# Kernel optimization log

Measured on AMD Instinct MI355X. Metric: run time of the kernel, lower is better.

Reference implementation:

```python
import jax, jax.numpy as jnp
import numpy as np

E, D, H, K = 8, 1024, 4096, 2  # num_experts, input/output dim, hidden dim, top-k
B, S = 2, 2048


def setup_inputs() -> dict:
    key = jax.random.key(0)
    ks = jax.random.split(key, 5)
    s = 0.02
    return {
        "x": jax.random.normal(ks[0], (B, S, D), dtype=jnp.float32),
        "router_w": jax.random.normal(ks[1], (D, E), dtype=jnp.float32) * s,
        "router_b": jnp.zeros((E,), jnp.float32),
        "w1": jax.random.normal(ks[2], (E, D, H), dtype=jnp.float32) * s,
        "b1": jnp.zeros((E, H), jnp.float32),
        "w2": jax.random.normal(ks[3], (E, H, D), dtype=jnp.float32) * s,
        "b2": jnp.zeros((E, D), jnp.float32),
        "gamma": jnp.ones((E, D), jnp.float32),
        "beta": jnp.zeros((E, D), jnp.float32),
    }


def _layernorm(y, g, b, eps=1e-5):
    mu = y.mean(-1, keepdims=True)
    var = ((y - mu) ** 2).mean(-1, keepdims=True)
    return (y - mu) * jax.lax.rsqrt(var + eps) * g + b


def reference(x, router_w, router_b, w1, b1, w2, b2, gamma, beta):
    # Router
    router_logits = x @ router_w + router_b            # [B,S,E]
    probs = jax.nn.softmax(router_logits, axis=-1)
    topk_p, topk_i = jax.lax.top_k(probs, K)           # [B,S,K]
    topk_p = topk_p / topk_p.sum(-1, keepdims=True)

    # All experts over all tokens (equivalent to the masked dense loop,
    # since every expert op is per-token). Dropout = identity (eval).
    h = jax.nn.gelu(jnp.einsum('bsd,edh->ebsh', x, w1) + b1[:, None, None, :],
                    approximate=False)                  # [E,B,S,H]
    y = jnp.einsum('ebsh,ehd->ebsd', h, w2) + b2[:, None, None, :]
    eo = _layernorm(y + x[None], gamma[:, None, None, :], beta[:, None, None, :])  # [E,B,S,D]

    # Combine top-k experts per token
    eo = jnp.moveaxis(eo, 0, 2)                         # [B,S,E,D]
    gathered = jnp.take_along_axis(eo, topk_i[..., None], axis=2)  # [B,S,K,D]
    output = (gathered * topk_p[..., None]).sum(axis=2)            # [B,S,D]
    return output, router_logits
```

## Files before the change

### kernel.cpp

```cpp
#include <hip/hip_runtime.h>
#include <math.h>

#define NE 8
#define DD 1024
#define HH 4096
#define TT 4096
#define RR 8192

typedef __attribute__((ext_vector_type(8))) short short8;
typedef __attribute__((ext_vector_type(4))) float f32x4;

__device__ __forceinline__ unsigned short f2bf(float f) {
    unsigned int u = __float_as_uint(f);
    u += 0x7fffu + ((u >> 16) & 1u);
    return (unsigned short)(u >> 16);
}

__device__ __forceinline__ float gelu_fast(float v) {
    float z = fabsf(v) * 0.70710678f;
    float t = __fdividef(1.0f, fmaf(0.3275911f, z, 1.0f));
    float p = fmaf(1.061405429f, t, -1.453152027f);
    p = fmaf(p, t, 1.421413741f);
    p = fmaf(p, t, -0.284496736f);
    p = fmaf(p, t, 0.254829592f);
    p = p * t;
    float erf = fmaf(-p, __expf(-z * z), 1.0f);
    return 0.5f * v * (1.0f + copysignf(erf, v));
}

__device__ __forceinline__ void async_copy16(void* lds, const void* g) {
    auto* lp = reinterpret_cast<__attribute__((address_space(3))) unsigned int*>(
        (unsigned int)(unsigned long long)(lds));
    auto* gp = reinterpret_cast<const __attribute__((address_space(1))) unsigned int*>(
        (unsigned long long)(g));
    __builtin_amdgcn_global_load_lds(gp, lp, 16, 0, 0);
}


__global__ void cvtx_kernel(const float* __restrict__ x, unsigned short* __restrict__ xb) {
    size_t i = (size_t)(blockIdx.x * 256 + threadIdx.x) * 4;
    float4 v = *(const float4*)&x[i];
    unsigned int lo = (unsigned int)f2bf(v.x) | ((unsigned int)f2bf(v.y) << 16);
    unsigned int hi = (unsigned int)f2bf(v.z) | ((unsigned int)f2bf(v.w) << 16);
    *(uint2*)&xb[i] = make_uint2(lo, hi);
}

__global__ __launch_bounds__(256) void transpose_swz_kernel(const float* __restrict__ src,
        unsigned short* __restrict__ dst, int K, int N) {
    const int e = blockIdx.z;
    src += (size_t)e * K * N;
    dst += (size_t)e * K * N;
    const int c0 = blockIdx.x * 64;
    const int r0 = blockIdx.y * 64;
    __shared__ unsigned short t[64][65];
    const int tid = threadIdx.x;
    const int rc4 = (tid & 15) * 4, rr = tid >> 4;
    #pragma unroll
    for (int i = 0; i < 4; i++) {
        int r = rr + i * 16;
        float4 v = *(const float4*)&src[(size_t)(r0 + r) * N + c0 + rc4];
        t[r][rc4]     = f2bf(v.x);
        t[r][rc4 + 1] = f2bf(v.y);
        t[r][rc4 + 2] = f2bf(v.z);
        t[r][rc4 + 3] = f2bf(v.w);
    }
    __syncthreads();
    const int n_local = tid & 63;
    const int n = c0 + n_local;
    const int nt = n >> 7, row = n & 127;
    const int Kdiv32 = K >> 5;
    #pragma unroll
    for (int it = 0; it < 2; it++) {
        int dg = (tid >> 6) + 4 * it;
        int kb = 2 * blockIdx.y + (dg >> 2);
        int q = dg & 3;
        unsigned short tmp[8];
        #pragma unroll
        for (int i = 0; i < 8; i++) tmp[i] = t[dg * 8 + i][n_local];
        size_t idx = ((((size_t)nt * Kdiv32 + kb) * 4 + q) * 128 + row) * 8;
        *(uint4*)&dst[idx] = *(uint4*)&tmp[0];
    }
}

__global__ void router_kernel(const float* __restrict__ x, const float* __restrict__ rw,
                              const float* __restrict__ rb, float* __restrict__ logits_out,
                              int* __restrict__ topk_e, float* __restrict__ topk_p,
                              int* __restrict__ counts) {
    const int t = blockIdx.x;
    const int tid = threadIdx.x;
    float4 xv = *(const float4*)&x[(size_t)t * DD + tid * 4];
    const float* rwp = rw + (size_t)(tid * 4) * NE;
    float acc[NE];
    #pragma unroll
    for (int e = 0; e < NE; e++) acc[e] = 0.f;
    float xs[4] = {xv.x, xv.y, xv.z, xv.w};
    #pragma unroll
    for (int i = 0; i < 4; i++) {
        #pragma unroll
        for (int e = 0; e < NE; e++) acc[e] += xs[i] * rwp[i * NE + e];
    }
    #pragma unroll
    for (int e = 0; e < NE; e++) {
        float v = acc[e];
        for (int off = 32; off > 0; off >>= 1) v += __shfl_down(v, off);
        acc[e] = v;
    }
    __shared__ float part[4][NE];
    if ((tid & 63) == 0) {
        #pragma unroll
        for (int e = 0; e < NE; e++) part[tid >> 6][e] = acc[e];
    }
    __syncthreads();
    if (tid == 0) {
        float lg[NE];
        #pragma unroll
        for (int e = 0; e < NE; e++)
            lg[e] = part[0][e] + part[1][e] + part[2][e] + part[3][e] + rb[e];
        #pragma unroll
        for (int e = 0; e < NE; e++) logits_out[(size_t)t * NE + e] = lg[e];
        float m = lg[0];
        #pragma unroll
        for (int e = 1; e < NE; e++) m = fmaxf(m, lg[e]);
        float pr[NE];
        #pragma unroll
        for (int e = 0; e < NE; e++) pr[e] = __expf(lg[e] - m);
        int i0 = 0;
        #pragma unroll
        for (int e = 1; e < NE; e++) if (pr[e] > pr[i0]) i0 = e;
        int i1 = (i0 == 0) ? 1 : 0;
        #pragma unroll
        for (int e = 0; e < NE; e++) if (e != i0 && pr[e] > pr[i1]) i1 = e;
        float p0 = pr[i0], p1 = pr[i1];
        float inv = 1.f / (p0 + p1);
        topk_e[t * 2] = i0;  topk_e[t * 2 + 1] = i1;
        topk_p[t * 2] = p0 * inv;  topk_p[t * 2 + 1] = p1 * inv;
        atomicAdd(&counts[i0], 1);
        atomicAdd(&counts[i1], 1);
    }
}

__global__ void prefix_kernel(const int* __restrict__ counts, int* __restrict__ offs,
                              int* __restrict__ cursor) {
    if (threadIdx.x == 0) {
        int a = 0;
        for (int e = 0; e < NE; e++) { offs[e] = a; cursor[e] = a; a += counts[e]; }
        offs[NE] = a;
    }
}

__global__ void scatter_kernel(const int* __restrict__ topk_e, int* __restrict__ cursor,
                               int* __restrict__ row_token, int* __restrict__ slot_of) {
    int i = blockIdx.x * 256 + threadIdx.x;
    int e = topk_e[i];
    int pos = atomicAdd(&cursor[e], 1);
    row_token[pos] = i >> 1;
    slot_of[i] = pos;
}

__device__ __forceinline__ void mfma_step(const unsigned short* Ab, const unsigned short* Bb,
        int wr, int wc, int m16, int q, f32x4 (&acc)[4][4]) {
    short8 af[4], bfr[4];
    #pragma unroll
    for (int i = 0; i < 4; i++) af[i] = *(const short8*)&Ab[q * 1024 + (wr + i * 16 + m16) * 8];
    #pragma unroll
    for (int j = 0; j < 4; j++) bfr[j] = *(const short8*)&Bb[q * 1024 + (wc + j * 16 + m16) * 8];
    #pragma unroll
    for (int i = 0; i < 4; i++)
        #pragma unroll
        for (int j = 0; j < 4; j++)
            acc[i][j] = __builtin_amdgcn_mfma_f32_16x16x32_bf16(af[i], bfr[j], acc[i][j], 0, 0, 0);
}

template <int NK>
__device__ __forceinline__ void kloop_db(
        const unsigned short* ag0, const unsigned short* ag1, const unsigned short* bg,
        unsigned short* As, unsigned short* Bs,
        int wv, int lane, int wr, int wc, int m16, int q, f32x4 (&acc)[4][4]) {
    unsigned short* alA = As + wv * 1024 + lane * 8;
    unsigned short* blB = Bs + wv * 1024 + lane * 8;

    async_copy16(alA, ag0);        async_copy16(alA + 512, ag1);
    async_copy16(blB, bg);         async_copy16(blB + 512, bg + 512);
    ag0 += 32; ag1 += 32; bg += 4096;

    #pragma unroll 1
    for (int it = 0; it < NK / 2 - 1; ++it) {
        async_copy16(alA + 4096, ag0); async_copy16(alA + 4608, ag1);
        async_copy16(blB + 4096, bg);  async_copy16(blB + 4608, bg + 512);
        ag0 += 32; ag1 += 32; bg += 4096;
        asm volatile("s_waitcnt vmcnt(4)" ::: "memory");
        __builtin_amdgcn_s_barrier();
        mfma_step(As, Bs, wr, wc, m16, q, acc);
        __builtin_amdgcn_s_barrier();
        async_copy16(alA, ag0);        async_copy16(alA + 512, ag1);
        async_copy16(blB, bg);         async_copy16(blB + 512, bg + 512);
        ag0 += 32; ag1 += 32; bg += 4096;
        asm volatile("s_waitcnt vmcnt(4)" ::: "memory");
        __builtin_amdgcn_s_barrier();
        mfma_step(As + 4096, Bs + 4096, wr, wc, m16, q, acc);
        __builtin_amdgcn_s_barrier();
    }
    async_copy16(alA + 4096, ag0); async_copy16(alA + 4608, ag1);
    async_copy16(blB + 4096, bg);  async_copy16(blB + 4608, bg + 512);
    asm volatile("s_waitcnt vmcnt(4)" ::: "memory");
    __builtin_amdgcn_s_barrier();
    mfma_step(As, Bs, wr, wc, m16, q, acc);
    asm volatile("s_waitcnt vmcnt(0)" ::: "memory");
    __builtin_amdgcn_s_barrier();
    mfma_step(As + 4096, Bs + 4096, wr, wc, m16, q, acc);
}

__global__ __launch_bounds__(256) void gemm1_kernel(
        const unsigned short* __restrict__ xb, const unsigned short* __restrict__ w1s,
        const float* __restrict__ b1, const int* __restrict__ offs,
        const int* __restrict__ row_token, unsigned short* __restrict__ hbuf) {
    const int bid = blockIdx.x;
    const int xcd = bid & 7;
    const int mem = (bid >> 3) & 7;
    const int g   = (bid >> 6) * 8 + xcd;
    const int nth = g & 3;
    const int rt  = (g >> 2) & 31;
    const int e   = g >> 7;
    const int nt  = nth * 8 + mem;

    const int r0 = offs[e];
    const int ne = offs[e + 1] - r0;
    if (rt * 128 >= ne) return;

    __shared__ __align__(16) unsigned short As[2][4096];
    __shared__ __align__(16) unsigned short Bs[2][4096];

    const int tid = threadIdx.x;
    const int lane = tid & 63;
    const int wv = tid >> 6;
    const int wr = (wv >> 1) * 64, wc = (wv & 1) * 64;
    const int m16 = lane & 15, q = lane >> 4;

    int ra = rt * 128 + lane;       ra = ra < ne ? ra : ne - 1;
    int rb = rt * 128 + 64 + lane;  rb = rb < ne ? rb : ne - 1;
    const unsigned short* ag0 = xb + (size_t)row_token[r0 + ra] * DD + wv * 8;
    const unsigned short* ag1 = xb + (size_t)row_token[r0 + rb] * DD + wv * 8;

    const unsigned short* bg = w1s + (size_t)e * HH * DD + (size_t)nt * (DD >> 5) * 4096
                               + wv * 1024 + lane * 8;

    f32x4 acc[4][4];
    f32x4 zero = {0.f, 0.f, 0.f, 0.f};
    #pragma unroll
    for (int i = 0; i < 4; i++)
        #pragma unroll
        for (int j = 0; j < 4; j++) acc[i][j] = zero;

    kloop_db<DD / 32>(ag0, ag1, bg, &As[0][0], &Bs[0][0], wv, lane, wr, wc, m16, q, acc);

    const int n0 = nt * 128;
    float b1v[4];
    #pragma unroll
    for (int j = 0; j < 4; j++) b1v[j] = b1[(size_t)e * HH + n0 + wc + j * 16 + m16];
    #pragma unroll
    for (int i = 0; i < 4; i++) {
        #pragma unroll
        for (int rg = 0; rg < 4; rg++) {
            int rr = rt * 128 + wr + i * 16 + q * 4 + rg;
            if (rr < ne) {
                unsigned short* hrow = hbuf + (size_t)(r0 + rr) * HH;
                #pragma unroll
                for (int j = 0; j < 4; j++) {
                    int col = n0 + wc + j * 16 + m16;
                    float v = acc[i][j][rg] + b1v[j];
                    hrow[col] = f2bf(gelu_fast(v));
                }
            }
        }
    }
}

__global__ __launch_bounds__(256) void gemm2_kernel(
        const unsigned short* __restrict__ hbuf, const unsigned short* __restrict__ w2s,
        const float* __restrict__ b2, const float* __restrict__ x,
        const int* __restrict__ offs, const int* __restrict__ row_token,
        float* __restrict__ yp0, float* __restrict__ yp1) {
    const int bid = blockIdx.x;
    const int xcd = bid & 7;
    const int nt  = (bid >> 3) & 7;
    const int g   = (bid >> 6) * 8 + xcd;
    const int chunk = g & 1;
    const int rt  = (g >> 1) & 31;
    const int e   = g >> 6;

    const int r0 = offs[e];
    const int ne = offs[e + 1] - r0;
    if (rt * 128 >= ne) return;
    const int kbase = chunk * (HH / 2);
    float* ybuf = chunk ? yp1 : yp0;

    __shared__ __align__(16) unsigned short As[2][4096];
    __shared__ __align__(16) unsigned short Bs[2][4096];

    const int tid = threadIdx.x;
    const int lane = tid & 63;
    const int wv = tid >> 6;
    const int wr = (wv >> 1) * 64, wc = (wv & 1) * 64;
    const int m16 = lane & 15, q = lane >> 4;

    int ra = rt * 128 + lane;       ra = ra < ne ? ra : ne - 1;
    int rb = rt * 128 + 64 + lane;  rb = rb < ne ? rb : ne - 1;
    const unsigned short* ag0 = hbuf + (size_t)(r0 + ra) * HH + kbase + wv * 8;
    const unsigned short* ag1 = hbuf + (size_t)(r0 + rb) * HH + kbase + wv * 8;

    const unsigned short* bg = w2s + (size_t)e * DD * HH + (size_t)nt * (HH >> 5) * 4096
                               + (size_t)(kbase >> 5) * 4096 + wv * 1024 + lane * 8;

    f32x4 acc[4][4];
    f32x4 zero = {0.f, 0.f, 0.f, 0.f};
    #pragma unroll
    for (int i = 0; i < 4; i++)
        #pragma unroll
        for (int j = 0; j < 4; j++) acc[i][j] = zero;

    kloop_db<(HH / 2) / 32>(ag0, ag1, bg, &As[0][0], &Bs[0][0], wv, lane, wr, wc, m16, q, acc);

    const int n0 = nt * 128;
    float b2v[4] = {0.f, 0.f, 0.f, 0.f};
    if (chunk == 0) {
        #pragma unroll
        for (int j = 0; j < 4; j++) b2v[j] = b2[(size_t)e * DD + n0 + wc + j * 16 + m16];
    }
    #pragma unroll
    for (int i = 0; i < 4; i++) {
        #pragma unroll
        for (int rg = 0; rg < 4; rg++) {
            int rr = rt * 128 + wr + i * 16 + q * 4 + rg;
            if (rr < ne) {
                float* yrow = ybuf + (size_t)(r0 + rr) * DD;
                if (chunk == 0) {
                    int tok = row_token[r0 + rr];
                    const float* xrow = x + (size_t)tok * DD;
                    #pragma unroll
                    for (int j = 0; j < 4; j++) {
                        int col = n0 + wc + j * 16 + m16;
                        yrow[col] = acc[i][j][rg] + b2v[j] + xrow[col];
                    }
                } else {
                    #pragma unroll
                    for (int j = 0; j < 4; j++) {
                        int col = n0 + wc + j * 16 + m16;
                        yrow[col] = acc[i][j][rg];
                    }
                }
            }
        }
    }
}

__global__ void ln_combine_kernel(const float* __restrict__ yp0, const float* __restrict__ yp1,
                                  const int* __restrict__ slot_of,
                                  const int* __restrict__ topk_e, const float* __restrict__ topk_p,
                                  const float* __restrict__ gamma, const float* __restrict__ beta,
                                  float* __restrict__ out) {
    const int t = blockIdx.x;
    const int tid = threadIdx.x;
    __shared__ float ps[8];
    float4 o = {0.f, 0.f, 0.f, 0.f};
    #pragma unroll
    for (int k = 0; k < 2; k++) {
        int row = slot_of[t * 2 + k];
        int e = topk_e[t * 2 + k];
        float p = topk_p[t * 2 + k];
        float4 v0 = *(const float4*)&yp0[(size_t)row * DD + tid * 4];
        float4 v1 = *(const float4*)&yp1[(size_t)row * DD + tid * 4];
        float4 v = {v0.x + v1.x, v0.y + v1.y, v0.z + v1.z, v0.w + v1.w};
        float s = v.x + v.y + v.z + v.w;
        float sq = v.x * v.x + v.y * v.y + v.z * v.z + v.w * v.w;
        for (int off = 32; off > 0; off >>= 1) {
            s += __shfl_down(s, off);
            sq += __shfl_down(sq, off);
        }
        if ((tid & 63) == 0) { ps[tid >> 6] = s; ps[4 + (tid >> 6)] = sq; }
        __syncthreads();
        float fs = ps[0] + ps[1] + ps[2] + ps[3];
        float fq = ps[4] + ps[5] + ps[6] + ps[7];
        float mu = fs * (1.0f / DD);
        float var = fq * (1.0f / DD) - mu * mu;
        float rsig = rsqrtf(var + 1e-5f);
        float4 g = *(const float4*)&gamma[(size_t)e * DD + tid * 4];
        float4 bb = *(const float4*)&beta[(size_t)e * DD + tid * 4];
        o.x += p * ((v.x - mu) * rsig * g.x + bb.x);
        o.y += p * ((v.y - mu) * rsig * g.y + bb.y);
        o.z += p * ((v.z - mu) * rsig * g.z + bb.z);
        o.w += p * ((v.w - mu) * rsig * g.w + bb.w);
        __syncthreads();
    }
    *(float4*)&out[(size_t)t * DD + tid * 4] = o;
}

extern "C" void kernel_launch(void* const* d_in, const int* in_sizes, int n_in,
                              void* d_out, int out_size, void* d_ws, size_t ws_size,
                              hipStream_t stream) {
    const float* x     = (const float*)d_in[0];
    const float* rw    = (const float*)d_in[1];
    const float* rb    = (const float*)d_in[2];
    const float* w1    = (const float*)d_in[3];
    const float* b1    = (const float*)d_in[4];
    const float* w2    = (const float*)d_in[5];
    const float* b2    = (const float*)d_in[6];
    const float* gamma = (const float*)d_in[7];
    const float* beta  = (const float*)d_in[8];

    float* out    = (float*)d_out;
    float* logits = out + (size_t)TT * DD;

    char* w = (char*)d_ws;
    int*   counts    = (int*)(w + 0);
    int*   offs      = (int*)(w + 64);
    int*   cursor    = (int*)(w + 128);
    int*   topk_e    = (int*)(w + 4096);
    float* topk_p    = (float*)(w + 36864);
    int*   row_token = (int*)(w + 69632);
    int*   slot_of   = (int*)(w + 102400);
    unsigned short* xb   = (unsigned short*)(w + (size_t)1 * 1048576);
    unsigned short* w1s  = (unsigned short*)(w + (size_t)9 * 1048576);
    unsigned short* w2s  = (unsigned short*)(w + (size_t)73 * 1048576);
    unsigned short* hbuf = (unsigned short*)(w + (size_t)137 * 1048576);
    float*          yp0  = (float*)(w + (size_t)1 * 1048576);
    float*          yp1  = (float*)(w + (size_t)33 * 1048576);

    hipMemsetAsync(w, 0, 1024, stream);

    transpose_swz_kernel<<<dim3(HH / 64, DD / 64, NE), 256, 0, stream>>>(w1, w1s, DD, HH);
    transpose_swz_kernel<<<dim3(DD / 64, HH / 64, NE), 256, 0, stream>>>(w2, w2s, HH, DD);
    cvtx_kernel<<<4096, 256, 0, stream>>>(x, xb);
    router_kernel<<<TT, 256, 0, stream>>>(x, rw, rb, logits, topk_e, topk_p, counts);
    prefix_kernel<<<1, 64, 0, stream>>>(counts, offs, cursor);
    scatter_kernel<<<RR / 256, 256, 0, stream>>>(topk_e, cursor, row_token, slot_of);
    gemm1_kernel<<<32 * 32 * NE, 256, 0, stream>>>(xb, w1s, b1, offs, row_token, hbuf);
    gemm2_kernel<<<16 * 32 * NE, 256, 0, stream>>>(hbuf, w2s, b2, x, offs, row_token, yp0, yp1);
    ln_combine_kernel<<<TT, 256, 0, stream>>>(yp0, yp1, slot_of, topk_e, topk_p, gamma, beta, out);
}
```

Measured before the change: 750.7 us.

## Use triple-buffered LDS pipeline and drop split-K in second GEMM

Replaces the double-buffered K loop with a three-stage async-copy ring buffer, so two tiles are in flight while one is being multiplied, which should hide more global-load latency. It also removes the two-way split-K in gemm2: each block now covers the full hidden dimension and writes a single y buffer, and ln_combine reads one partial instead of two. This cuts the fp32 partial-buffer traffic, but it halves gemm2's grid and raises LDS use per block (48KB), which may reduce occupancy and parallelism.

```diff
diff --git a/kernel.cpp b/kernel.cpp
--- a/kernel.cpp
+++ b/kernel.cpp
@@ -172,42 +172,41 @@
 }
 
 template <int NK>
-__device__ __forceinline__ void kloop_db(
+__device__ __forceinline__ void kloop_3s(
         const unsigned short* ag0, const unsigned short* ag1, const unsigned short* bg,
         unsigned short* As, unsigned short* Bs,
         int wv, int lane, int wr, int wc, int m16, int q, f32x4 (&acc)[4][4]) {
     unsigned short* alA = As + wv * 1024 + lane * 8;
     unsigned short* blB = Bs + wv * 1024 + lane * 8;
 
-    async_copy16(alA, ag0);        async_copy16(alA + 512, ag1);
-    async_copy16(blB, bg);         async_copy16(blB + 512, bg + 512);
-    ag0 += 32; ag1 += 32; bg += 4096;
-
+    #pragma unroll
+    for (int p = 0; p < 2; ++p) {
+        async_copy16(alA + p * 4096, ag0); async_copy16(alA + p * 4096 + 512, ag1);
+        async_copy16(blB + p * 4096, bg);  async_copy16(blB + p * 4096 + 512, bg + 512);
+        ag0 += 32; ag1 += 32; bg += 4096;
+    }
+
+    int cOff = 0;
+    int sOff = 2 * 4096;
     #pragma unroll 1
-    for (int it = 0; it < NK / 2 - 1; ++it) {
-        async_copy16(alA + 4096, ag0); async_copy16(alA + 4608, ag1);
-        async_copy16(blB + 4096, bg);  async_copy16(blB + 4608, bg + 512);
+    for (int t = 0; t < NK - 2; ++t) {
+        async_copy16(alA + sOff, ag0); async_copy16(alA + sOff + 512, ag1);
+        async_copy16(blB + sOff, bg);  async_copy16(blB + sOff + 512, bg + 512);
         ag0 += 32; ag1 += 32; bg += 4096;
-        asm volatile("s_waitcnt vmcnt(4)" ::: "memory");
+        asm volatile("s_waitcnt vmcnt(8)" ::: "memory");
         __builtin_amdgcn_s_barrier();
-        mfma_step(As, Bs, wr, wc, m16, q, acc);
+        mfma_step(As + cOff, Bs + cOff, wr, wc, m16, q, acc);
         __builtin_amdgcn_s_barrier();
-        async_copy16(alA, ag0);        async_copy16(alA + 512, ag1);
-        async_copy16(blB, bg);         async_copy16(blB + 512, bg + 512);
-        ag0 += 32; ag1 += 32; bg += 4096;
-        asm volatile("s_waitcnt vmcnt(4)" ::: "memory");
-        __builtin_amdgcn_s_barrier();
-        mfma_step(As + 4096, Bs + 4096, wr, wc, m16, q, acc);
-        __builtin_amdgcn_s_barrier();
-    }
-    async_copy16(alA + 4096, ag0); async_copy16(alA + 4608, ag1);
-    async_copy16(blB + 4096, bg);  async_copy16(blB + 4608, bg + 512);
+        sOff = cOff;
+        cOff += 4096; if (cOff == 3 * 4096) cOff = 0;
+    }
     asm volatile("s_waitcnt vmcnt(4)" ::: "memory");
     __builtin_amdgcn_s_barrier();
-    mfma_step(As, Bs, wr, wc, m16, q, acc);
+    mfma_step(As + cOff, Bs + cOff, wr, wc, m16, q, acc);
+    cOff += 4096; if (cOff == 3 * 4096) cOff = 0;
     asm volatile("s_waitcnt vmcnt(0)" ::: "memory");
     __builtin_amdgcn_s_barrier();
-    mfma_step(As + 4096, Bs + 4096, wr, wc, m16, q, acc);
+    mfma_step(As + cOff, Bs + cOff, wr, wc, m16, q, acc);
 }
 
 __global__ __launch_bounds__(256) void gemm1_kernel(
@@ -227,8 +226,8 @@
     const int ne = offs[e + 1] - r0;
     if (rt * 128 >= ne) return;
 
-    __shared__ __align__(16) unsigned short As[2][4096];
-    __shared__ __align__(16) unsigned short Bs[2][4096];
+    __shared__ __align__(16) unsigned short As[3][4096];
+    __shared__ __align__(16) unsigned short Bs[3][4096];
 
     const int tid = threadIdx.x;
     const int lane = tid & 63;
@@ -251,7 +250,7 @@
         #pragma unroll
         for (int j = 0; j < 4; j++) acc[i][j] = zero;
 
-    kloop_db<DD / 32>(ag0, ag1, bg, &As[0][0], &Bs[0][0], wv, lane, wr, wc, m16, q, acc);
+    kloop_3s<DD / 32>(ag0, ag1, bg, &As[0][0], &Bs[0][0], wv, lane, wr, wc, m16, q, acc);
 
     const int n0 = nt * 128;
     float b1v[4];
@@ -279,23 +278,20 @@
         const unsigned short* __restrict__ hbuf, const unsigned short* __restrict__ w2s,
         const float* __restrict__ b2, const float* __restrict__ x,
         const int* __restrict__ offs, const int* __restrict__ row_token,
-        float* __restrict__ yp0, float* __restrict__ yp1) {
+        float* __restrict__ yp) {
     const int bid = blockIdx.x;
     const int xcd = bid & 7;
     const int nt  = (bid >> 3) & 7;
     const int g   = (bid >> 6) * 8 + xcd;
-    const int chunk = g & 1;
-    const int rt  = (g >> 1) & 31;
-    const int e   = g >> 6;
+    const int rt  = g & 31;
+    const int e   = g >> 5;
 
     const int r0 = offs[e];
     const int ne = offs[e + 1] - r0;
     if (rt * 128 >= ne) return;
-    const int kbase = chunk * (HH / 2);
-    float* ybuf = chunk ? yp1 : yp0;
-
-    __shared__ __align__(16) unsigned short As[2][4096];
-    __shared__ __align__(16) unsigned short Bs[2][4096];
+
+    __shared__ __align__(16) unsigned short As[3][4096];
+    __shared__ __align__(16) unsigned short Bs[3][4096];
 
     const int tid = threadIdx.x;
     const int lane = tid & 63;
@@ -305,11 +301,11 @@
 
     int ra = rt * 128 + lane;       ra = ra < ne ? ra : ne - 1;
     int rb = rt * 128 + 64 + lane;  rb = rb < ne ? rb : ne - 1;
-    const unsigned short* ag0 = hbuf + (size_t)(r0 + ra) * HH + kbase + wv * 8;
-    const unsigned short* ag1 = hbuf + (size_t)(r0 + rb) * HH + kbase + wv * 8;
+    const unsigned short* ag0 = hbuf + (size_t)(r0 + ra) * HH + wv * 8;
+    const unsigned short* ag1 = hbuf + (size_t)(r0 + rb) * HH + wv * 8;
 
     const unsigned short* bg = w2s + (size_t)e * DD * HH + (size_t)nt * (HH >> 5) * 4096
-                               + (size_t)(kbase >> 5) * 4096 + wv * 1024 + lane * 8;
+                               + wv * 1024 + lane * 8;
 
     f32x4 acc[4][4];
     f32x4 zero = {0.f, 0.f, 0.f, 0.f};
@@ -318,42 +314,32 @@
         #pragma unroll
         for (int j = 0; j < 4; j++) acc[i][j] = zero;
 
-    kloop_db<(HH / 2) / 32>(ag0, ag1, bg, &As[0][0], &Bs[0][0], wv, lane, wr, wc, m16, q, acc);
+    kloop_3s<HH / 32>(ag0, ag1, bg, &As[0][0], &Bs[0][0], wv, lane, wr, wc, m16, q, acc);
 
     const int n0 = nt * 128;
-    float b2v[4] = {0.f, 0.f, 0.f, 0.f};
-    if (chunk == 0) {
-        #pragma unroll
-        for (int j = 0; j < 4; j++) b2v[j] = b2[(size_t)e * DD + n0 + wc + j * 16 + m16];
-    }
+    float b2v[4];
+    #pragma unroll
+    for (int j = 0; j < 4; j++) b2v[j] = b2[(size_t)e * DD + n0 + wc + j * 16 + m16];
     #pragma unroll
     for (int i = 0; i < 4; i++) {
         #pragma unroll
         for (int rg = 0; rg < 4; rg++) {
             int rr = rt * 128 + wr + i * 16 + q * 4 + rg;
             if (rr < ne) {
-                float* yrow = ybuf + (size_t)(r0 + rr) * DD;
-                if (chunk == 0) {
-                    int tok = row_token[r0 + rr];
-                    const float* xrow = x + (size_t)tok * DD;
-                    #pragma unroll
-                    for (int j = 0; j < 4; j++) {
-                        int col = n0 + wc + j * 16 + m16;
-                        yrow[col] = acc[i][j][rg] + b2v[j] + xrow[col];
-                    }
-                } else {
-                    #pragma unroll
-                    for (int j = 0; j < 4; j++) {
-                        int col = n0 + wc + j * 16 + m16;
-                        yrow[col] = acc[i][j][rg];
-                    }
+                float* yrow = yp + (size_t)(r0 + rr) * DD;
+                int tok = row_token[r0 + rr];
+                const float* xrow = x + (size_t)tok * DD;
+                #pragma unroll
+                for (int j = 0; j < 4; j++) {
+                    int col = n0 + wc + j * 16 + m16;
+                    yrow[col] = acc[i][j][rg] + b2v[j] + xrow[col];
                 }
             }
         }
     }
 }
 
-__global__ void ln_combine_kernel(const float* __restrict__ yp0, const float* __restrict__ yp1,
+__global__ void ln_combine_kernel(const float* __restrict__ yp,
                                   const int* __restrict__ slot_of,
                                   const int* __restrict__ topk_e, const float* __restrict__ topk_p,
                                   const float* __restrict__ gamma, const float* __restrict__ beta,
@@ -367,9 +353,7 @@
         int row = slot_of[t * 2 + k];
         int e = topk_e[t * 2 + k];
         float p = topk_p[t * 2 + k];
-        float4 v0 = *(const float4*)&yp0[(size_t)row * DD + tid * 4];
-        float4 v1 = *(const float4*)&yp1[(size_t)row * DD + tid * 4];
-        float4 v = {v0.x + v1.x, v0.y + v1.y, v0.z + v1.z, v0.w + v1.w};
+        float4 v = *(const float4*)&yp[(size_t)row * DD + tid * 4];
         float s = v.x + v.y + v.z + v.w;
         float sq = v.x * v.x + v.y * v.y + v.z * v.z + v.w * v.w;
         for (int off = 32; off > 0; off >>= 1) {
@@ -422,8 +406,7 @@
     unsigned short* w1s  = (unsigned short*)(w + (size_t)9 * 1048576);
     unsigned short* w2s  = (unsigned short*)(w + (size_t)73 * 1048576);
     unsigned short* hbuf = (unsigned short*)(w + (size_t)137 * 1048576);
-    float*          yp0  = (float*)(w + (size_t)1 * 1048576);
-    float*          yp1  = (float*)(w + (size_t)33 * 1048576);
+    float*          yp   = (float*)(w + (size_t)1 * 1048576);
 
     hipMemsetAsync(w, 0, 1024, stream);
 
@@ -434,6 +417,6 @@
     prefix_kernel<<<1, 64, 0, stream>>>(counts, offs, cursor);
     scatter_kernel<<<RR / 256, 256, 0, stream>>>(topk_e, cursor, row_token, slot_of);
     gemm1_kernel<<<32 * 32 * NE, 256, 0, stream>>>(xb, w1s, b1, offs, row_token, hbuf);
-    gemm2_kernel<<<16 * 32 * NE, 256, 0, stream>>>(hbuf, w2s, b2, x, offs, row_token, yp0, yp1);
-    ln_combine_kernel<<<TT, 256, 0, stream>>>(yp0, yp1, slot_of, topk_e, topk_p, gamma, beta, out);
-}
+    gemm2_kernel<<<8 * 32 * NE, 256, 0, stream>>>(hbuf, w2s, b2, x, offs, row_token, yp);
+    ln_combine_kernel<<<TT, 256, 0, stream>>>(yp, slot_of, topk_e, topk_p, gamma, beta, out);
+}
```

Measured after the change: 765.1 us. No clear change (+1.9%).
